# Performance work log

Hardware: AMD Instinct MI355X
Metric: run time of the kernel (lower is better)

Reference implementation:

```python
import jax, jax.numpy as jnp
import numpy as np

N = 50000   # nodes
E = 200000  # edges per snapshot
T = 2       # temporal snapshots
IN = 64     # in_dim
H = 32      # h_dim
ED = 16     # edge_dim
Z = 32      # z_dim
S = 5       # neighbor samples


def setup_inputs() -> dict:
    key = jax.random.key(0)
    ks = jax.random.split(key, 20)
    g = lambda i, shape: jax.random.normal(ks[i], shape, jnp.float32) * 0.05
    return {
        "x": jax.random.normal(ks[0], (N, IN), jnp.float32),
        "ei0": jax.random.randint(ks[1], (2, E), 0, N, dtype=jnp.int32),
        "ea0": jax.random.normal(ks[2], (E, ED), jnp.float32),
        "ei1": jax.random.randint(ks[3], (2, E), 0, N, dtype=jnp.int32),
        "ea1": jax.random.normal(ks[4], (E, ED), jnp.float32),
        "idx": jnp.sort(jax.random.randint(ks[5], (N + 1,), 0, E, dtype=jnp.int32)),
        "ptr": jax.random.randint(ks[6], (E,), 0, N, dtype=jnp.int32),
        "W1": g(7, (IN, H)), "b1": jnp.zeros((H,), jnp.float32),
        "W2": g(8, (H, H)), "b2": jnp.zeros((H,), jnp.float32),
        "W3": g(9, (H, H)), "b3": jnp.zeros((H,), jnp.float32),
        "nnW1": g(10, (ED, 8)), "nnb1": jnp.zeros((8,), jnp.float32),
        "nnW2": g(11, (8, H * H)), "nnb2": jnp.zeros((H * H,), jnp.float32),
        "root": g(12, (H, H)), "cbias": jnp.zeros((H,), jnp.float32),
        "Wih": g(13, (3 * H, H)), "Whh": g(14, (3 * H, H)),
        "bih": jnp.zeros((3 * H,), jnp.float32), "bhh": jnp.zeros((3 * H,), jnp.float32),
        "Wlin": g(15, (H, Z)), "blin": jnp.zeros((Z,), jnp.float32),
        "Wdec": g(16, (Z, Z)), "bdec": jnp.zeros((Z,), jnp.float32),
    }


def _gcn(z, src, dst, W, b):
    # GCNConv with symmetric norm; self loops already in (src, dst)
    deg = jax.ops.segment_sum(jnp.ones_like(src, jnp.float32), dst, N)
    dinv = jnp.where(deg > 0, 1.0 / jnp.sqrt(jnp.maximum(deg, 1.0)), 0.0)
    h = z @ W
    msg = (dinv[src] * dinv[dst])[:, None] * h[src]
    return jax.ops.segment_sum(msg, dst, N) + b


def _nnconv(z, src, dst, ea, nnW1, nnb1, nnW2, nnb2, root, cbias):
    # edge MLP -> per-edge [H,H] weight, per-edge matvec, mean-scatter at dst
    We = (jax.nn.relu(ea @ nnW1 + nnb1) @ nnW2 + nnb2).reshape(-1, H, H)
    msg = jnp.einsum('eh,eho->eo', z[src], We)
    cnt = jax.ops.segment_sum(jnp.ones_like(src, jnp.float32), dst, N)
    agg = jax.ops.segment_sum(msg, dst, N) / jnp.maximum(cnt, 1.0)[:, None]
    return agg + z @ root + cbias


def _forward(x, ei0, ea0, ei1, ea1, idx, ptr,
             W1, b1, W2, b2, W3, b3, nnW1, nnb1, nnW2, nnb2, root, cbias,
             Wih, Whh, bih, bhh, Wlin, blin, Wdec, bdec):
    loops = jnp.arange(N, dtype=ei0.dtype)

    def snap(ei, ea):
        src, dst = ei[0], ei[1]
        ssl = jnp.concatenate([src, loops])
        dsl = jnp.concatenate([dst, loops])
        z = _gcn(x, ssl, dsl, W1, b1)                 # c1 (no act)
        z = jax.nn.relu(_gcn(z, ssl, dsl, W2, b2))    # c2 + relu (dropout=eval)
        z = jax.nn.relu(_gcn(z, ssl, dsl, W3, b3))    # c3 + relu
        return jnp.tanh(_nnconv(z, src, dst, ea, nnW1, nnb1, nnW2, nnb2, root, cbias))

    zs = jnp.stack([snap(ei0, ea0), snap(ei1, ea1)], axis=1)  # [N, T, H]

    # nn.GRU(batch_first=False) on [N, T, H]: scans over NODE axis, batch=T
    def step(h, xt):
        gi = xt @ Wih.T + bih
        gh = h @ Whh.T + bhh
        ir, iz, inn = jnp.split(gi, 3, axis=-1)
        hr, hz, hn = jnp.split(gh, 3, axis=-1)
        r = jax.nn.sigmoid(ir + hr)
        u = jax.nn.sigmoid(iz + hz)
        n = jnp.tanh(inn + r * hn)
        hnew = (1.0 - u) * n + u * h
        return hnew, hnew

    _, ys = jax.lax.scan(step, jnp.zeros((T, H), jnp.float32), zs)
    out = ys @ Wlin + blin  # [N, T, Z]

    # sample_z: uniform sample of S neighbors (with replacement) from CSR (idx, ptr)
    deg = (idx[1:] - idx[:-1]).astype(jnp.float32)  # [N]
    key = jax.random.key(42)
    res = []
    for t in range(T):
        u = jax.random.uniform(jax.random.fold_in(key, t), (N, S))
        j = jnp.floor(u * deg[:, None]).astype(idx.dtype)
        pos = jnp.clip(idx[:-1, None] + j, 0, E - 1)
        nb = ptr[pos]                               # [N, S] sampled neighbors
        zt = out[:, t, :]
        ag = (zt[nb].sum(axis=1) + zt) / (S + 1.0)
        ag = jnp.where((deg > 0)[:, None], ag, zt)  # no neighbors -> identity
        res.append(jax.nn.softmax(ag @ Wdec + bdec, axis=1))
    return jnp.stack(res)  # [T, N, Z]


def reference(x, ei0, ea0, ei1, ea1, idx, ptr,
              W1, b1, W2, b2, W3, b3, nnW1, nnb1, nnW2, nnb2, root, cbias,
              Wih, Whh, bih, bhh, Wlin, blin, Wdec, bdec):
    return _forward(x, ei0, ea0, ei1, ea1, idx, ptr,
                    W1, b1, W2, b2, W3, b3, nnW1, nnb1, nnW2, nnb2, root, cbias,
                    Wih, Whh, bih, bhh, Wlin, blin, Wdec, bdec)
```

## Files before the change

kernel.cpp:

```cpp
#include <hip/hip_runtime.h>
#include <stdint.h>

constexpr int NN = 50000;
constexpr int EE = 200000;
constexpr int N2 = 2*NN;
constexpr int E2 = 2*EE;
constexpr int GRU_WARM   = 16;
constexpr int GRU_CHUNKS = 3072;
constexpr int NB_SCAN = (N2 + 511) / 512;

#define DEVI __device__ __forceinline__

typedef float f32x2 __attribute__((ext_vector_type(2)));

DEVI uint32_t rotl32(uint32_t v, int d){ return (v<<d)|(v>>(32-d)); }

#define TFR(r) { x0 += x1; x1 = rotl32(x1, r); x1 ^= x0; }
DEVI void tf2x32(uint32_t k0, uint32_t k1, uint32_t x0, uint32_t x1,
                 uint32_t& o0, uint32_t& o1){
  uint32_t ks2 = k0 ^ k1 ^ 0x1BD11BDAu;
  x0 += k0; x1 += k1;
  TFR(13) TFR(15) TFR(26) TFR(6)
  x0 += k1;  x1 += ks2 + 1u;
  TFR(17) TFR(29) TFR(16) TFR(24)
  x0 += ks2; x1 += k0 + 2u;
  TFR(13) TFR(15) TFR(26) TFR(6)
  x0 += k0;  x1 += k1 + 3u;
  TFR(17) TFR(29) TFR(16) TFR(24)
  x0 += k1;  x1 += ks2 + 4u;
  TFR(13) TFR(15) TFR(26) TFR(6)
  x0 += ks2; x1 += k0 + 5u;
  o0 = x0; o1 = x1;
}

DEVI unsigned short bfr(float f){
  uint32_t u = __float_as_uint(f);
  return (unsigned short)((u + 0x7fffu + ((u >> 16) & 1u)) >> 16);
}
DEVI float bfi(unsigned short h){ return __uint_as_float(((uint32_t)h) << 16); }

DEVI uint32_t pk4f8(float a, float b, float c, float d){
  int r = 0;
  r = __builtin_amdgcn_cvt_pk_fp8_f32(a, b, r, false);
  r = __builtin_amdgcn_cvt_pk_fp8_f32(c, d, r, true);
  return (uint32_t)r;
}
DEVI float4 upk4f8(uint32_t u){
  f32x2 lo = __builtin_amdgcn_cvt_pk_f32_fp8((int)u, false);
  f32x2 hi = __builtin_amdgcn_cvt_pk_f32_fp8((int)u, true);
  return make_float4(lo.x, lo.y, hi.x, hi.y);
}
constexpr float P8SCALE = 64.0f;

template<int K, int ACTIN, int TRW, int EPI>
__global__ __launch_bounds__(256) void tgemm_k(
    const float* __restrict__ X, const float* __restrict__ Wg,
    const float* __restrict__ Bv, float* __restrict__ Y, float* __restrict__ Y2,
    const float* __restrict__ dinvB, unsigned short* __restrict__ Ybf,
    int rows, int Mt, int wld){
  __shared__ float xt[K*132];
  __shared__ float wl[K*32];
  const int gr = blockIdx.x, gy = blockIdx.y;
  #pragma unroll
  for (int p=0; p<K/8; p++){
    int flat = p*256 + threadIdx.x;
    int row  = flat / (K/4);
    int kq   = flat % (K/4);
    int grow = min(gr*128 + row, rows-1);
    float4 v = *(const float4*)(X + (size_t)grow*K + kq*4);
    if (ACTIN){ v.x=fmaxf(v.x,0.f); v.y=fmaxf(v.y,0.f); v.z=fmaxf(v.z,0.f); v.w=fmaxf(v.w,0.f); }
    xt[(kq*4+0)*132 + row] = v.x;
    xt[(kq*4+1)*132 + row] = v.y;
    xt[(kq*4+2)*132 + row] = v.z;
    xt[(kq*4+3)*132 + row] = v.w;
  }
  for (int i=threadIdx.x; i<K*32; i+=256){
    int k = i >> 5, c = i & 31;
    wl[i] = TRW ? Wg[(size_t)(gy*32+c)*wld + k] : Wg[(size_t)k*wld + gy*32 + c];
  }
  __syncthreads();
  const int tr4 = (threadIdx.x & 31) << 2;
  const int tc4 = (threadIdx.x >> 5) << 2;
  float acc[4][4] = {};
  #pragma unroll 8
  for (int k=0; k<K; k++){
    const float4 xv = *(const float4*)(xt + k*132 + tr4);
    const float4 wv = *(const float4*)(wl + (k<<5) + tc4);
    acc[0][0]=fmaf(xv.x,wv.x,acc[0][0]); acc[0][1]=fmaf(xv.x,wv.y,acc[0][1]);
    acc[0][2]=fmaf(xv.x,wv.z,acc[0][2]); acc[0][3]=fmaf(xv.x,wv.w,acc[0][3]);
    acc[1][0]=fmaf(xv.y,wv.x,acc[1][0]); acc[1][1]=fmaf(xv.y,wv.y,acc[1][1]);
    acc[1][2]=fmaf(xv.y,wv.z,acc[1][2]); acc[1][3]=fmaf(xv.y,wv.w,acc[1][3]);
    acc[2][0]=fmaf(xv.z,wv.x,acc[2][0]); acc[2][1]=fmaf(xv.z,wv.y,acc[2][1]);
    acc[2][2]=fmaf(xv.z,wv.z,acc[2][2]); acc[2][3]=fmaf(xv.z,wv.w,acc[2][3]);
    acc[3][0]=fmaf(xv.w,wv.x,acc[3][0]); acc[3][1]=fmaf(xv.w,wv.y,acc[3][1]);
    acc[3][2]=fmaf(xv.w,wv.z,acc[3][2]); acc[3][3]=fmaf(xv.w,wv.w,acc[3][3]);
  }
  const int cbase = gy*32 + tc4;
  float b4[4] = {0,0,0,0};
  if (Bv){ b4[0]=Bv[cbase]; b4[1]=Bv[cbase+1]; b4[2]=Bv[cbase+2]; b4[3]=Bv[cbase+3]; }
  #pragma unroll
  for (int i=0;i<4;i++){
    int r = gr*128 + tr4 + i;
    if (r >= rows) break;
    if (EPI == 0){
      float4 o = { acc[i][0]+b4[0], acc[i][1]+b4[1], acc[i][2]+b4[2], acc[i][3]+b4[3] };
      *(float4*)(Y + (size_t)r*Mt + cbase) = o;
    } else if (EPI == 1){
      float dv = dinvB[r];
      float4 hs = { dv*acc[i][0], dv*acc[i][1], dv*acc[i][2], dv*acc[i][3] };
      ushort4 u = { bfr(hs.x), bfr(hs.y), bfr(hs.z), bfr(hs.w) };
      *(ushort4*)(Ybf + ((size_t)r<<5) + tc4) = u;
      float4 o = { b4[0]+dv*hs.x, b4[1]+dv*hs.y, b4[2]+dv*hs.z, b4[3]+dv*hs.w };
      *(float4*)(Y2 + ((size_t)r<<5) + tc4) = o;
    } else if (EPI == 2){
      ushort4 u = { bfr(acc[i][0]+b4[0]), bfr(acc[i][1]+b4[1]),
                    bfr(acc[i][2]+b4[2]), bfr(acc[i][3]+b4[3]) };
      *(ushort4*)(Ybf + (size_t)r*Mt + cbase) = u;
    } else {
      #pragma unroll
      for (int s=0;s<2;s++){
        int rr = r*2+s;
        float dv = dinvB[rr];
        float4 hs = { dv*acc[i][0], dv*acc[i][1], dv*acc[i][2], dv*acc[i][3] };
        ushort4 u = { bfr(hs.x), bfr(hs.y), bfr(hs.z), bfr(hs.w) };
        *(ushort4*)(Ybf + ((size_t)rr<<5) + tc4) = u;
        float4 o = { b4[0]+dv*hs.x, b4[1]+dv*hs.y, b4[2]+dv*hs.z, b4[3]+dv*hs.w };
        *(float4*)(Y2 + ((size_t)rr<<5) + tc4) = o;
      }
    }
  }
}

__global__ __launch_bounds__(256) void pgemm_k(const float* __restrict__ X,
    const float* __restrict__ Wbig2, unsigned char* __restrict__ P8,
    float* __restrict__ R, int rows){
  __shared__ float xt[32*132];
  __shared__ float wl[32*160];
  const int gr = blockIdx.x, gh = blockIdx.y;
  #pragma unroll
  for (int p=0; p<4; p++){
    int flat = p*256 + threadIdx.x;
    int row = flat >> 3, kq = flat & 7;
    int grow = min(gr*128 + row, rows-1);
    float4 v = *(const float4*)(X + (size_t)grow*32 + kq*4);
    v.x=fmaxf(v.x,0.f); v.y=fmaxf(v.y,0.f); v.z=fmaxf(v.z,0.f); v.w=fmaxf(v.w,0.f);
    xt[(kq*4+0)*132 + row] = v.x;
    xt[(kq*4+1)*132 + row] = v.y;
    xt[(kq*4+2)*132 + row] = v.z;
    xt[(kq*4+3)*132 + row] = v.w;
  }
  for (int i=threadIdx.x; i<(32*160/4); i+=256){
    int k = i / 40, c4 = i - k*40;
    ((float4*)wl)[i] = ((const float4*)Wbig2)[k*80 + gh*40 + c4];
  }
  __syncthreads();
  const int tr4 = (threadIdx.x & 31) << 2;
  const int tc4 = (threadIdx.x >> 5) << 2;
  for (int g=0; g<5; g++){
    int sg = gh*5 + g;
    float acc[4][4] = {};
    #pragma unroll 8
    for (int k=0; k<32; k++){
      const float4 xv = *(const float4*)(xt + k*132 + tr4);
      const float4 wv = *(const float4*)(wl + k*160 + g*32 + tc4);
      acc[0][0]=fmaf(xv.x,wv.x,acc[0][0]); acc[0][1]=fmaf(xv.x,wv.y,acc[0][1]);
      acc[0][2]=fmaf(xv.x,wv.z,acc[0][2]); acc[0][3]=fmaf(xv.x,wv.w,acc[0][3]);
      acc[1][0]=fmaf(xv.y,wv.x,acc[1][0]); acc[1][1]=fmaf(xv.y,wv.y,acc[1][1]);
      acc[1][2]=fmaf(xv.y,wv.z,acc[1][2]); acc[1][3]=fmaf(xv.y,wv.w,acc[1][3]);
      acc[2][0]=fmaf(xv.z,wv.x,acc[2][0]); acc[2][1]=fmaf(xv.z,wv.y,acc[2][1]);
      acc[2][2]=fmaf(xv.z,wv.z,acc[2][2]); acc[2][3]=fmaf(xv.z,wv.w,acc[2][3]);
      acc[3][0]=fmaf(xv.w,wv.x,acc[3][0]); acc[3][1]=fmaf(xv.w,wv.y,acc[3][1]);
      acc[3][2]=fmaf(xv.w,wv.z,acc[3][2]); acc[3][3]=fmaf(xv.w,wv.w,acc[3][3]);
    }
    #pragma unroll
    for (int i=0;i<4;i++){
      int r = gr*128 + tr4 + i;
      if (r >= rows) break;
      if (sg < 9){
        uint32_t u = pk4f8(acc[i][0]*P8SCALE, acc[i][1]*P8SCALE,
                           acc[i][2]*P8SCALE, acc[i][3]*P8SCALE);
        *(uint32_t*)(P8 + (size_t)r*288 + sg*32 + tc4) = u;
      } else {
        float4 o = { acc[i][0], acc[i][1], acc[i][2], acc[i][3] };
        *(float4*)(R + ((size_t)r<<5) + tc4) = o;
      }
    }
  }
}

__global__ __launch_bounds__(256) void gigemm_k(const float* __restrict__ X,
    const float* __restrict__ Wih, const float* __restrict__ bih,
    unsigned short* __restrict__ gi16, int rows){
  __shared__ float xt[32*132];
  __shared__ float wl[32*96];
  const int gr = blockIdx.x;
  #pragma unroll
  for (int p=0; p<4; p++){
    int flat = p*256 + threadIdx.x;
    int row = flat >> 3, kq = flat & 7;
    int grow = min(gr*128 + row, rows-1);
    float4 v = *(const float4*)(X + (size_t)grow*32 + kq*4);
    xt[(kq*4+0)*132 + row] = v.x;
    xt[(kq*4+1)*132 + row] = v.y;
    xt[(kq*4+2)*132 + row] = v.z;
    xt[(kq*4+3)*132 + row] = v.w;
  }
  for (int i=threadIdx.x; i<32*96; i+=256){
    int k = i / 96, c = i - k*96;
    wl[i] = Wih[(size_t)c*32 + k];
  }
  __syncthreads();
  const int tr4 = (threadIdx.x & 31) << 2;
  const int tc4 = (threadIdx.x >> 5) << 2;
  for (int g=0; g<3; g++){
    float acc[4][4] = {};
    #pragma unroll 8
    for (int k=0; k<32; k++){
      const float4 xv = *(const float4*)(xt + k*132 + tr4);
      const float4 wv = *(const float4*)(wl + k*96 + g*32 + tc4);
      acc[0][0]=fmaf(xv.x,wv.x,acc[0][0]); acc[0][1]=fmaf(xv.x,wv.y,acc[0][1]);
      acc[0][2]=fmaf(xv.x,wv.z,acc[0][2]); acc[0][3]=fmaf(xv.x,wv.w,acc[0][3]);
      acc[1][0]=fmaf(xv.y,wv.x,acc[1][0]); acc[1][1]=fmaf(xv.y,wv.y,acc[1][1]);
      acc[1][2]=fmaf(xv.y,wv.z,acc[1][2]); acc[1][3]=fmaf(xv.y,wv.w,acc[1][3]);
      acc[2][0]=fmaf(xv.z,wv.x,acc[2][0]); acc[2][1]=fmaf(xv.z,wv.y,acc[2][1]);
      acc[2][2]=fmaf(xv.z,wv.z,acc[2][2]); acc[2][3]=fmaf(xv.z,wv.w,acc[2][3]);
      acc[3][0]=fmaf(xv.w,wv.x,acc[3][0]); acc[3][1]=fmaf(xv.w,wv.y,acc[3][1]);
      acc[3][2]=fmaf(xv.w,wv.z,acc[3][2]); acc[3][3]=fmaf(xv.w,wv.w,acc[3][3]);
    }
    const int cbase = g*32 + tc4;
    const float4 b4 = *(const float4*)(bih + cbase);
    #pragma unroll
    for (int i=0;i<4;i++){
      int r = gr*128 + tr4 + i;
      if (r >= rows) break;
      ushort4 u = { bfr(acc[i][0]+b4.x), bfr(acc[i][1]+b4.y),
                    bfr(acc[i][2]+b4.z), bfr(acc[i][3]+b4.w) };
      *(ushort4*)(gi16 + (size_t)r*96 + cbase) = u;
    }
  }
}

__global__ __launch_bounds__(512) void scan1_k(const int* __restrict__ cnt,
                                               int* __restrict__ loc, int* __restrict__ bsum){
  int tid = threadIdx.x;
  int i = blockIdx.x*512 + tid;
  int v = (i < N2) ? cnt[i] : 0;
  int lane = tid & 63, w = tid >> 6;
  int s = v;
  #pragma unroll
  for (int d=1; d<64; d<<=1){ int o = __shfl_up(s, d); if (lane >= d) s += o; }
  __shared__ int wsum[8];
  if (lane == 63) wsum[w] = s;
  __syncthreads();
  int add = 0;
  #pragma unroll
  for (int k=0;k<8;k++) if (k < w) add += wsum[k];
  if (i < N2) loc[i] = add + s - v;
  if (tid == 511) bsum[blockIdx.x] = add + s;
}

__global__ __launch_bounds__(256) void scan2_k(int* __restrict__ bsum){
  int tid = threadIdx.x;
  int v = (tid < NB_SCAN) ? bsum[tid] : 0;
  int lane = tid & 63, w = tid >> 6;
  int s = v;
  #pragma unroll
  for (int d=1; d<64; d<<=1){ int o = __shfl_up(s, d); if (lane >= d) s += o; }
  __shared__ int wsum[4];
  if (lane == 63) wsum[w] = s;
  __syncthreads();
  int add = 0;
  #pragma unroll
  for (int k=0;k<4;k++) if (k < w) add += wsum[k];
  if (tid < NB_SCAN) bsum[tid] = add + s - v;
}

__global__ void scan3_k(const int* __restrict__ bsum, int* __restrict__ cursor,
                        int* __restrict__ rowptr, const int* __restrict__ cnt,
                        float* __restrict__ dinvB, float* __restrict__ degB){
  int i = blockIdx.x*blockDim.x + threadIdx.x;
  if (i < N2){
    int r = cursor[i] + bsum[i >> 9];
    rowptr[i] = r; cursor[i] = r;
    float c = (float)cnt[i];
    degB[i] = c; dinvB[i] = rsqrtf(c + 1.0f);
  }
  if (i == N2) rowptr[N2] = E2;
}

__global__ void fill_k(const int* __restrict__ ei0, const int* __restrict__ ei1,
                       int* __restrict__ cursor,
                       int* __restrict__ csr_src, int* __restrict__ csr_eid){
  int t = blockIdx.x*blockDim.x + threadIdx.x;
  if (t >= E2) return;
  int s = t >= EE;
  const int* ei = s ? ei1 : ei0;
  int e = t - s*EE;
  int d = ei[EE + e];
  int slot = atomicAdd(cursor + d*2 + s, 1);
  csr_src[slot] = ei[e]*2 + s;
  csr_eid[slot] = e;
}

__global__ __launch_bounds__(256) void temlp_k(const float* __restrict__ ea0,
    const float* __restrict__ ea1, const int* __restrict__ ei0,
    const int* __restrict__ ei1, const float* __restrict__ nnW1,
    const float* __restrict__ nnb1, unsigned short* __restrict__ tb,
    int* __restrict__ cnt){
  __shared__ float wt[136];
  for (int i=threadIdx.x; i<136; i+=256)
    wt[i] = (i < 128) ? nnW1[(i & 15)*8 + (i >> 4)] : nnb1[i - 128];
  __syncthreads();
  int t = blockIdx.x*256 + threadIdx.x;
  if (t >= E2) return;
  int s = t >= EE;
  const float* ea = s ? ea1 : ea0;
  const int*   ei = s ? ei1 : ei0;
  int e = t - s*EE;
  atomicAdd(cnt + ei[EE + e]*2 + s, 1);
  const float4 a0 = *(const float4*)(ea + (size_t)e*16);
  const float4 a1 = *(const float4*)(ea + (size_t)e*16 + 4);
  const float4 a2 = *(const float4*)(ea + (size_t)e*16 + 8);
  const float4 a3 = *(const float4*)(ea + (size_t)e*16 + 12);
  unsigned short o8[8];
  #pragma unroll
  for (int m=0;m<8;m++){
    const float* wc = wt + m*16;
    float v = wt[128+m];
    v = fmaf(a0.x,wc[0], fmaf(a0.y,wc[1], fmaf(a0.z,wc[2], fmaf(a0.w,wc[3], v))));
    v = fmaf(a1.x,wc[4], fmaf(a1.y,wc[5], fmaf(a1.z,wc[6], fmaf(a1.w,wc[7], v))));
    v = fmaf(a2.x,wc[8], fmaf(a2.y,wc[9], fmaf(a2.z,wc[10],fmaf(a2.w,wc[11],v))));
    v = fmaf(a3.x,wc[12],fmaf(a3.y,wc[13],fmaf(a3.z,wc[14],fmaf(a3.w,wc[15],v))));
    o8[m] = bfr(fmaxf(v, 0.0f));
  }
  ushort4* tp = (ushort4*)(tb + (size_t)t*8);
  tp[0] = make_ushort4(o8[0],o8[1],o8[2],o8[3]);
  tp[1] = make_ushort4(o8[4],o8[5],o8[6],o8[7]);
}

__global__ __launch_bounds__(256) void gcngath_k(const unsigned short* __restrict__ hs,
    const float* __restrict__ dinvB, const int* __restrict__ rowptr,
    const int* __restrict__ csr_src, float* __restrict__ out){
  int t = blockIdx.x*256 + threadIdx.x;
  int n = t >> 3;
  if (n >= N2) return;
  int q = (t & 7) << 2;
  int b = rowptr[n], e = rowptr[n+1];
  float4 acc = {0,0,0,0};
  int p = b;
  for (; p + 2 <= e; p += 2){
    int s0 = csr_src[p], s1 = csr_src[p+1];
    ushort4 h0 = *(const ushort4*)(hs + ((size_t)s0<<5) + q);
    ushort4 h1 = *(const ushort4*)(hs + ((size_t)s1<<5) + q);
    acc.x += bfi(h0.x) + bfi(h1.x);
    acc.y += bfi(h0.y) + bfi(h1.y);
    acc.z += bfi(h0.z) + bfi(h1.z);
    acc.w += bfi(h0.w) + bfi(h1.w);
  }
  if (p < e){
    int s0 = csr_src[p];
    ushort4 h0 = *(const ushort4*)(hs + ((size_t)s0<<5) + q);
    acc.x += bfi(h0.x); acc.y += bfi(h0.y); acc.z += bfi(h0.z); acc.w += bfi(h0.w);
  }
  float dv = dinvB[n];
  float4 o = *(float4*)(out + ((size_t)n<<5) + q);
  o.x += dv*acc.x; o.y += dv*acc.y; o.z += dv*acc.z; o.w += dv*acc.w;
  *(float4*)(out + ((size_t)n<<5) + q) = o;
}

__global__ __launch_bounds__(256) void nngath_k(const unsigned char* __restrict__ P8,
    const unsigned short* __restrict__ tb,
    const int* __restrict__ rowptr, const int* __restrict__ csr_src,
    const int* __restrict__ csr_eid, float* __restrict__ R,
    const float* __restrict__ degB, const float* __restrict__ cbias){
  int t = blockIdx.x*256 + threadIdx.x;
  int n = t >> 3;
  if (n >= N2) return;
  int lane8 = threadIdx.x & 7;
  int ob = lane8 << 2;
  int sEE = (n & 1) ? EE : 0;
  int b = rowptr[n], e = rowptr[n+1];
  float4 acc = {0,0,0,0};
  int p = b;
  for (; p + 2 <= e; p += 2){
    int v0 = csr_src[p],   e0 = csr_eid[p];
    int v1 = csr_src[p+1], e1 = csr_eid[p+1];
    const unsigned char* pr0 = P8 + (size_t)v0*288 + ob;
    const unsigned char* pr1 = P8 + (size_t)v1*288 + ob;
    uint32_t u0[9], u1[9];
    #pragma unroll
    for (int k=0;k<9;k++) u0[k] = *(const uint32_t*)(pr0 + k*32);
    #pragma unroll
    for (int k=0;k<9;k++) u1[k] = *(const uint32_t*)(pr1 + k*32);
    ushort4 ta0 = *(const ushort4*)(tb + (size_t)(sEE + e0)*8);
    ushort4 tb0 = *(const ushort4*)(tb + (size_t)(sEE + e0)*8 + 4);
    ushort4 ta1 = *(const ushort4*)(tb + (size_t)(sEE + e1)*8);
    ushort4 tb1 = *(const ushort4*)(tb + (size_t)(sEE + e1)*8 + 4);
    float tc0[8] = { bfi(ta0.x),bfi(ta0.y),bfi(ta0.z),bfi(ta0.w),
                     bfi(tb0.x),bfi(tb0.y),bfi(tb0.z),bfi(tb0.w) };
    float tc1[8] = { bfi(ta1.x),bfi(ta1.y),bfi(ta1.z),bfi(ta1.w),
                     bfi(tb1.x),bfi(tb1.y),bfi(tb1.z),bfi(tb1.w) };
    float4 m0 = upk4f8(u0[0]);
    float4 m1 = upk4f8(u1[0]);
    #pragma unroll
    for (int k=0;k<8;k++){
      float4 q0 = upk4f8(u0[k+1]);
      m0.x = fmaf(tc0[k], q0.x, m0.x);
      m0.y = fmaf(tc0[k], q0.y, m0.y);
      m0.z = fmaf(tc0[k], q0.z, m0.z);
      m0.w = fmaf(tc0[k], q0.w, m0.w);
      float4 q1 = upk4f8(u1[k+1]);
      m1.x = fmaf(tc1[k], q1.x, m1.x);
      m1.y = fmaf(tc1[k], q1.y, m1.y);
      m1.z = fmaf(tc1[k], q1.z, m1.z);
      m1.w = fmaf(tc1[k], q1.w, m1.w);
    }
    acc.x += m0.x + m1.x; acc.y += m0.y + m1.y;
    acc.z += m0.z + m1.z; acc.w += m0.w + m1.w;
  }
  if (p < e){
    int v0 = csr_src[p], e0 = csr_eid[p];
    const unsigned char* pr0 = P8 + (size_t)v0*288 + ob;
    uint32_t u0[9];
    #pragma unroll
    for (int k=0;k<9;k++) u0[k] = *(const uint32_t*)(pr0 + k*32);
    ushort4 ta0 = *(const ushort4*)(tb + (size_t)(sEE + e0)*8);
    ushort4 tb0 = *(const ushort4*)(tb + (size_t)(sEE + e0)*8 + 4);
    float tc0[8] = { bfi(ta0.x),bfi(ta0.y),bfi(ta0.z),bfi(ta0.w),
                     bfi(tb0.x),bfi(tb0.y),bfi(tb0.z),bfi(tb0.w) };
    float4 m0 = upk4f8(u0[0]);
    #pragma unroll
    for (int k=0;k<8;k++){
      float4 q0 = upk4f8(u0[k+1]);
      m0.x = fmaf(tc0[k], q0.x, m0.x);
      m0.y = fmaf(tc0[k], q0.y, m0.y);
      m0.z = fmaf(tc0[k], q0.z, m0.z);
      m0.w = fmaf(tc0[k], q0.w, m0.w);
    }
    acc.x += m0.x; acc.y += m0.y; acc.z += m0.z; acc.w += m0.w;
  }
  float inv = (1.0f/P8SCALE) / fmaxf(degB[n], 1.0f);
  float4 rv = *(const float4*)(R + ((size_t)n<<5) + ob);
  const float4 cb = *(const float4*)(cbias + ob);
  float4 v;
  v.x = rv.x + cb.x + acc.x*inv;
  v.y = rv.y + cb.y + acc.y*inv;
  v.z = rv.z + cb.z + acc.z*inv;
  v.w = rv.w + cb.w + acc.w*inv;
  float4 o;
  o.x = 1.0f - 2.0f/(__expf(2.0f*v.x)+1.0f);
  o.y = 1.0f - 2.0f/(__expf(2.0f*v.y)+1.0f);
  o.z = 1.0f - 2.0f/(__expf(2.0f*v.z)+1.0f);
  o.w = 1.0f - 2.0f/(__expf(2.0f*v.w)+1.0f);
  *(float4*)(R + ((size_t)n<<5) + ob) = o;
}

__global__ void wprep_k(const float* __restrict__ nnW2, const float* __restrict__ nnb2,
                        const float* __restrict__ root,
                        const float* __restrict__ Wlin, const float* __restrict__ blin,
                        const float* __restrict__ Wdec, const float* __restrict__ bdec,
                        float* __restrict__ Wbig2, float* __restrict__ Wp,
                        float* __restrict__ bp){
  int i = blockIdx.x*blockDim.x + threadIdx.x;
  if (i < 32*320){
    int j = i / 320, m = i - j*320;
    float v;
    if (m >= 288)      v = root[j*32 + (m - 288)];
    else { int k = m >> 5, o = m & 31;
           v = (k == 0) ? nnb2[j*32 + o] : nnW2[(size_t)(k-1)*1024 + j*32 + o]; }
    Wbig2[i] = v;
  } else if (i < 32*320 + 1024){
    int ii = i - 32*320;
    int k = ii >> 5, m = ii & 31;
    float s = 0.0f;
    #pragma unroll 8
    for (int j=0;j<32;j++) s = fmaf(Wlin[k*32+j], Wdec[j*32+m], s);
    Wp[ii] = s;
  } else if (i < 32*320 + 1056){
    int m = i - 32*320 - 1024;
    float s = bdec[m];
    #pragma unroll 8
    for (int j=0;j<32;j++) s = fmaf(blin[j], Wdec[j*32+m], s);
    bp[m] = s;
  }
}

__global__ __launch_bounds__(64) __attribute__((amdgpu_waves_per_eu(3)))
void gru_k(const unsigned short* __restrict__ gi16,
    const float* __restrict__ Whh, const float* __restrict__ bhh,
    float* __restrict__ ys, int L){
  __shared__ float hl[64];
  int lane = threadIdx.x;
  int j = lane & 31, t = lane >> 5;
  int start = blockIdx.x * L;
  if (start >= NN) return;
  int end = min(start + L, NN);
  int n0 = max(0, start - GRU_WARM);
  float wr[32], wz[32], wn[32];
  #pragma unroll
  for (int k=0;k<32;k++) wr[k] = Whh[j*32 + k];
  #pragma unroll
  for (int k=0;k<32;k++) wz[k] = Whh[(32+j)*32 + k];
  #pragma unroll
  for (int k=0;k<32;k++) wn[k] = Whh[(64+j)*32 + k];
  #pragma unroll
  for (int k=0;k<32;k++)
    asm volatile("" : "+v"(wr[k]), "+v"(wz[k]), "+v"(wn[k]));
  float br = bhh[j], bz = bhh[32+j], bn = bhh[64+j];
  float h = 0.0f;
  hl[lane] = 0.0f;
  const unsigned short* g0 = gi16 + ((size_t)n0*2 + t)*96;
  float c0 = bfi(g0[j]), c1 = bfi(g0[32+j]), c2 = bfi(g0[64+j]);
  const float* hb = hl + (t << 5);
  for (int n = n0; n < end; n++){
    int np = (n+1 < end) ? n+1 : n;
    const unsigned short* gp = gi16 + ((size_t)np*2 + t)*96;
    float p0 = bfi(gp[j]), p1 = bfi(gp[32+j]), p2 = bfi(gp[64+j]);
    float ar = br, az = bz, an = bn;
    #pragma unroll
    for (int kk=0; kk<8; kk++){
      const float4 h4 = *(const float4*)(hb + (kk<<2));
      ar = fmaf(h4.x, wr[kk*4+0], ar); az = fmaf(h4.x, wz[kk*4+0], az); an = fmaf(h4.x, wn[kk*4+0], an);
      ar = fmaf(h4.y, wr[kk*4+1], ar); az = fmaf(h4.y, wz[kk*4+1], az); an = fmaf(h4.y, wn[kk*4+1], an);
      ar = fmaf(h4.z, wr[kk*4+2], ar); az = fmaf(h4.z, wz[kk*4+2], az); an = fmaf(h4.z, wn[kk*4+2], an);
      ar = fmaf(h4.w, wr[kk*4+3], ar); az = fmaf(h4.w, wz[kk*4+3], az); an = fmaf(h4.w, wn[kk*4+3], an);
    }
    float r = 1.0f/(1.0f + __expf(-(c0+ar)));
    float u = 1.0f/(1.0f + __expf(-(c1+az)));
    float pre = c2 + r*an;
    float e2 = __expf(2.0f*pre);
    float nn2 = 1.0f - 2.0f/(e2 + 1.0f);
    h = (1.0f-u)*nn2 + u*h;
    hl[lane] = h;
    if (n >= start) ys[((size_t)n << 6) + lane] = h;
    c0 = p0; c1 = p1; c2 = p2;
  }
}

__global__ __launch_bounds__(256) void final_k(const unsigned short* __restrict__ Lp,
    const int* __restrict__ idx, const int* __restrict__ ptr,
    float* __restrict__ dout){
  int grp = blockIdx.x*8 + (threadIdx.x >> 5);
  if (grp >= N2) return;
  int o = threadIdx.x & 31;
  int lane = threadIdx.x & 63;
  int t = (grp >= NN) ? 1 : 0;
  int n = grp - (t ? NN : 0);
  int i0 = idx[n], i1 = idx[n+1];
  float degf = (float)(i1 - i0);
  int nb = 0;
  {
    uint32_t fk0, fk1;
    tf2x32(0u, 42u, 0u, (uint32_t)t, fk0, fk1);
    int sidx = (o < 5) ? o : 4;
    uint32_t b = (uint32_t)(n*5 + sidx);
    bool hi = (b >= 125000u);
    uint32_t pair = hi ? (b - 125000u) : b;
    uint32_t r0, r1;
    tf2x32(fk0, fk1, pair, pair + 125000u, r0, r1);
    uint32_t bits = hi ? r1 : r0;
    float u = __uint_as_float((bits >> 9) | 0x3f800000u) - 1.0f;
    int jj = (int)floorf(u * degf);
    int pos = i0 + jj;
    pos = min(max(pos, 0), EE - 1);
    nb = ptr[pos];
  }
  float lo = bfi(Lp[((size_t)(n*2 + t) << 5) + o]);
  if (degf > 0.0f){
    float ssum = lo;
    #pragma unroll
    for (int s5=0;s5<5;s5++){
      int ns = __shfl(nb, (lane & 32) | s5);
      ssum += bfi(Lp[((size_t)(ns*2 + t) << 5) + o]);
    }
    lo = ssum * (1.0f/6.0f);
  }
  float m = lo;
  #pragma unroll
  for (int d5=16; d5>0; d5>>=1) m = fmaxf(m, __shfl_xor(m, d5));
  float ex = __expf(lo - m);
  float sum = ex;
  #pragma unroll
  for (int d5=16; d5>0; d5>>=1) sum += __shfl_xor(sum, d5);
  dout[((size_t)t*NN + n)*32 + o] = ex / sum;
}

static inline int g256(int n){ return (n + 255) / 256; }

extern "C" void kernel_launch(void* const* d_in, const int* in_sizes, int n_in,
                              void* d_out, int out_size, void* d_ws, size_t ws_size,
                              hipStream_t stream){
  const float* x    = (const float*)d_in[0];
  const int*   ei0  = (const int*)  d_in[1];
  const float* ea0  = (const float*)d_in[2];
  const int*   ei1  = (const int*)  d_in[3];
  const float* ea1  = (const float*)d_in[4];
  const int*   idx  = (const int*)  d_in[5];
  const int*   ptr  = (const int*)  d_in[6];
  const float* W1   = (const float*)d_in[7];
  const float* b1   = (const float*)d_in[8];
  const float* W2   = (const float*)d_in[9];
  const float* b2   = (const float*)d_in[10];
  const float* W3   = (const float*)d_in[11];
  const float* b3   = (const float*)d_in[12];
  const float* nnW1 = (const float*)d_in[13];
  const float* nnb1 = (const float*)d_in[14];
  const float* nnW2 = (const float*)d_in[15];
  const float* nnb2 = (const float*)d_in[16];
  const float* root = (const float*)d_in[17];
  const float* cbias= (const float*)d_in[18];
  const float* Wih  = (const float*)d_in[19];
  const float* Whh  = (const float*)d_in[20];
  const float* bih  = (const float*)d_in[21];
  const float* bhh  = (const float*)d_in[22];
  const float* Wlin = (const float*)d_in[23];
  const float* blin = (const float*)d_in[24];
  const float* Wdec = (const float*)d_in[25];
  const float* bdec = (const float*)d_in[26];

  float* ws = (float*)d_ws;
  size_t off = 0;
  float* degB = ws + off; off += N2;
  float* dinvB= ws + off; off += N2;
  float* Wbig2= ws + off; off += 32*320;
  float* Wp   = ws + off; off += 1024;
  float* bp   = ws + off; off += 32;
  int*   ib   = (int*)(ws + off); off += 1200000;
  unsigned short* tbuf = (unsigned short*)(ws + off); off += 1600000;
  float* A    = ws + off; off += (size_t)N2*32;
  float* B    = ws + off; off += (size_t)N2*32;
  float* C    = ws + off; off += (size_t)N2*32;
  float* D    = ws + off; off += (size_t)N2*80;
  unsigned short* hbf = (unsigned short*)D;
  unsigned char*  P8  = (unsigned char*)D;
  unsigned short* gi16 = (unsigned short*)B;
  float* ys   = D;
  unsigned short* Lp = (unsigned short*)A;

  int* cnt     = ib;
  int* rowptr  = ib + N2;
  int* cursor  = ib + 2*N2 + 1;
  int* bsum    = ib + 3*N2 + 1;
  int* csr_src = ib + 3*N2 + 1 + 256;
  int* csr_eid = csr_src + E2;

  const dim3 gN1(( NN + 127)/128, 1);
  const dim3 gB1((N2 + 127)/128, 1);
  const dim3 gP2((N2 + 127)/128, 2);

  wprep_k<<<g256(32*320 + 1056), 256, 0, stream>>>(nnW2, nnb2, root, Wlin, blin,
                                                   Wdec, bdec, Wbig2, Wp, bp);
  hipMemsetAsync(cnt, 0, N2*sizeof(int), stream);
  temlp_k<<<g256(E2), 256, 0, stream>>>(ea0, ea1, ei0, ei1, nnW1, nnb1, tbuf, cnt);
  scan1_k<<<NB_SCAN, 512, 0, stream>>>(cnt, cursor, bsum);
  scan2_k<<<1, 256, 0, stream>>>(bsum);
  scan3_k<<<g256(N2+1), 256, 0, stream>>>(bsum, cursor, rowptr, cnt, dinvB, degB);
  fill_k<<<g256(E2), 256, 0, stream>>>(ei0, ei1, cursor, csr_src, csr_eid);

  tgemm_k<64,0,0,4><<<gN1, 256, 0, stream>>>(x, W1, b1, nullptr, B, dinvB, hbf, NN, 32, 32);
  gcngath_k<<<g256(N2*8), 256, 0, stream>>>(hbf, dinvB, rowptr, csr_src, B);
  tgemm_k<32,0,0,1><<<gB1, 256, 0, stream>>>(B, W2, b2, nullptr, C, dinvB, hbf, N2, 32, 32);
  gcngath_k<<<g256(N2*8), 256, 0, stream>>>(hbf, dinvB, rowptr, csr_src, C);
  tgemm_k<32,1,0,1><<<gB1, 256, 0, stream>>>(C, W3, b3, nullptr, B, dinvB, hbf, N2, 32, 32);
  gcngath_k<<<g256(N2*8), 256, 0, stream>>>(hbf, dinvB, rowptr, csr_src, B);
  pgemm_k<<<gP2, 256, 0, stream>>>(B, Wbig2, P8, A, N2);
  nngath_k<<<g256(N2*8), 256, 0, stream>>>(P8, tbuf, rowptr, csr_src, csr_eid, A, degB, cbias);
  gigemm_k<<<gB1, 256, 0, stream>>>(A, Wih, bih, gi16, N2);
  int L = (NN + GRU_CHUNKS - 1) / GRU_CHUNKS;
  gru_k<<<GRU_CHUNKS, 64, 0, stream>>>(gi16, Whh, bhh, ys, L);
  tgemm_k<32,0,0,2><<<gB1, 256, 0, stream>>>(ys, Wp, bp, nullptr, nullptr, nullptr, Lp, N2, 32, 32);
  final_k<<<(N2 + 7)/8, 256, 0, stream>>>(Lp, idx, ptr, (float*)d_out);
}
```

Before: 302.1 us.

## Split GRU recurrence per timestep across blocks with half-K lane reduction

The GRU kernel now gives each block a single snapshot (t) instead of both. The two half-waves each take half of the 32-wide hidden dot product and combine their partial sums with a cross-half shuffle. This halves per-thread weight registers (48 instead of 96) and doubles the number of blocks, so more waves can be resident. Chunk count drops from 3072 to 2048, making each sequential chunk longer (fewer warm-up overheads) but lengthening the serial chain per block. The added shuffles sit on the recurrence's critical path.

```diff
diff --git a/kernel.cpp b/kernel.cpp
--- a/kernel.cpp
+++ b/kernel.cpp
@@ -6,7 +6,7 @@
 constexpr int N2 = 2*NN;
 constexpr int E2 = 2*EE;
 constexpr int GRU_WARM   = 16;
-constexpr int GRU_CHUNKS = 3072;
+constexpr int GRU_CHUNKS = 2048;
 constexpr int NB_SCAN = (N2 + 511) / 512;
 
 #define DEVI __device__ __forceinline__
@@ -485,54 +485,59 @@
   }
 }
 
-__global__ __launch_bounds__(64) __attribute__((amdgpu_waves_per_eu(3)))
+__global__ __launch_bounds__(64) __attribute__((amdgpu_waves_per_eu(1, 4)))
 void gru_k(const unsigned short* __restrict__ gi16,
     const float* __restrict__ Whh, const float* __restrict__ bhh,
     float* __restrict__ ys, int L){
-  __shared__ float hl[64];
+  __shared__ float hl[32];
   int lane = threadIdx.x;
-  int j = lane & 31, t = lane >> 5;
-  int start = blockIdx.x * L;
+  int j = lane & 31, hf = lane >> 5;
+  int chunk = blockIdx.x >> 1, t = blockIdx.x & 1;
+  int start = chunk * L;
   if (start >= NN) return;
   int end = min(start + L, NN);
   int n0 = max(0, start - GRU_WARM);
-  float wr[32], wz[32], wn[32];
-  #pragma unroll
-  for (int k=0;k<32;k++) wr[k] = Whh[j*32 + k];
-  #pragma unroll
-  for (int k=0;k<32;k++) wz[k] = Whh[(32+j)*32 + k];
-  #pragma unroll
-  for (int k=0;k<32;k++) wn[k] = Whh[(64+j)*32 + k];
-  #pragma unroll
-  for (int k=0;k<32;k++)
-    asm volatile("" : "+v"(wr[k]), "+v"(wz[k]), "+v"(wn[k]));
+  const int kb = hf << 4;
+  float wr[16], wz[16], wn[16];
+  #pragma unroll
+  for (int k=0;k<16;k++) wr[k] = Whh[j*32 + kb + k];
+  #pragma unroll
+  for (int k=0;k<16;k++) wz[k] = Whh[(32+j)*32 + kb + k];
+  #pragma unroll
+  for (int k=0;k<16;k++) wn[k] = Whh[(64+j)*32 + kb + k];
   float br = bhh[j], bz = bhh[32+j], bn = bhh[64+j];
   float h = 0.0f;
-  hl[lane] = 0.0f;
+  if (lane < 32) hl[lane] = 0.0f;
   const unsigned short* g0 = gi16 + ((size_t)n0*2 + t)*96;
   float c0 = bfi(g0[j]), c1 = bfi(g0[32+j]), c2 = bfi(g0[64+j]);
-  const float* hb = hl + (t << 5);
+  const float* hb = hl + kb;
   for (int n = n0; n < end; n++){
     int np = (n+1 < end) ? n+1 : n;
     const unsigned short* gp = gi16 + ((size_t)np*2 + t)*96;
     float p0 = bfi(gp[j]), p1 = bfi(gp[32+j]), p2 = bfi(gp[64+j]);
-    float ar = br, az = bz, an = bn;
-    #pragma unroll
-    for (int kk=0; kk<8; kk++){
+    float ar = 0.0f, az = 0.0f, an = 0.0f;
+    #pragma unroll
+    for (int kk=0; kk<4; kk++){
       const float4 h4 = *(const float4*)(hb + (kk<<2));
       ar = fmaf(h4.x, wr[kk*4+0], ar); az = fmaf(h4.x, wz[kk*4+0], az); an = fmaf(h4.x, wn[kk*4+0], an);
       ar = fmaf(h4.y, wr[kk*4+1], ar); az = fmaf(h4.y, wz[kk*4+1], az); an = fmaf(h4.y, wn[kk*4+1], an);
       ar = fmaf(h4.z, wr[kk*4+2], ar); az = fmaf(h4.z, wz[kk*4+2], az); an = fmaf(h4.z, wn[kk*4+2], an);
       ar = fmaf(h4.w, wr[kk*4+3], ar); az = fmaf(h4.w, wz[kk*4+3], az); an = fmaf(h4.w, wn[kk*4+3], an);
     }
+    ar += __shfl_xor(ar, 32);
+    az += __shfl_xor(az, 32);
+    an += __shfl_xor(an, 32);
+    ar += br; az += bz; an += bn;
     float r = 1.0f/(1.0f + __expf(-(c0+ar)));
     float u = 1.0f/(1.0f + __expf(-(c1+az)));
     float pre = c2 + r*an;
     float e2 = __expf(2.0f*pre);
     float nn2 = 1.0f - 2.0f/(e2 + 1.0f);
     h = (1.0f-u)*nn2 + u*h;
-    hl[lane] = h;
-    if (n >= start) ys[((size_t)n << 6) + lane] = h;
+    if (lane < 32){
+      hl[lane] = h;
+      if (n >= start) ys[((size_t)n << 6) + t*32 + j] = h;
+    }
     c0 = p0; c1 = p1; c2 = p2;
   }
 }
@@ -667,7 +672,7 @@
   nngath_k<<<g256(N2*8), 256, 0, stream>>>(P8, tbuf, rowptr, csr_src, csr_eid, A, degB, cbias);
   gigemm_k<<<gB1, 256, 0, stream>>>(A, Wih, bih, gi16, N2);
   int L = (NN + GRU_CHUNKS - 1) / GRU_CHUNKS;
-  gru_k<<<GRU_CHUNKS, 64, 0, stream>>>(gi16, Whh, bhh, ys, L);
+  gru_k<<<GRU_CHUNKS*2, 64, 0, stream>>>(gi16, Whh, bhh, ys, L);
   tgemm_k<32,0,0,2><<<gB1, 256, 0, stream>>>(ys, Wp, bp, nullptr, nullptr, nullptr, Lp, N2, 32, 32);
   final_k<<<(N2 + 7)/8, 256, 0, stream>>>(Lp, idx, ptr, (float*)d_out);
 }
```

New measurement: 299.7 us. About the same (-0.8%).
